# Kernel optimization log

Hardware: AMD Instinct MI355X
Metric: run time of the kernel (lower is better)

## Reference

```python
import jax, jax.numpy as jnp
import numpy as np

B, DIM, H, HD, DS = 256, 1024, 16, 64, 4
NL, NKV = HD, HD * DS  # mask shape constraint: num_tok_q == head_dim, num_tok_kv == head_dim*downscaling
EPS = 1e-5


def _ln(t, g, b):
    m = t.mean(-1, keepdims=True)
    v = ((t - m) ** 2).mean(-1, keepdims=True)
    return (t - m) / jnp.sqrt(v + EPS) * g + b


def setup_inputs() -> dict:
    key = jax.random.key(0)
    ks = jax.random.split(key, 7)
    s = DIM ** -0.5
    return {
        'x': jax.random.normal(ks[0], (B, NKV, DIM), jnp.float32),
        'latents': jax.random.normal(ks[1], (B, NL, DIM), jnp.float32),
        'Wq': jax.random.normal(ks[2], (DIM, DIM), jnp.float32) * s,
        'Wk': jax.random.normal(ks[3], (DIM, DIM), jnp.float32) * s,
        'Wv': jax.random.normal(ks[4], (DIM, DIM), jnp.float32) * s,
        'Wo': jax.random.normal(ks[5], (DIM, DIM), jnp.float32) * s,
        'bo': jnp.zeros((DIM,), jnp.float32),
        'g_out': jnp.ones((DIM,), jnp.float32),
        'b_out': jnp.zeros((DIM,), jnp.float32),
        'g_x': jnp.ones((DIM,), jnp.float32),
        'b_x': jnp.zeros((DIM,), jnp.float32),
        'g_l': jnp.ones((DIM,), jnp.float32),
        'b_l': jnp.zeros((DIM,), jnp.float32),
    }


def reference(x, latents, Wq, Wk, Wv, Wo, bo, g_out, b_out, g_x, b_x, g_l, b_l):
    # pre-norms
    ln_l = _ln(latents, g_l, b_l)   # (B, NL, DIM) -> queries
    ln_x = _ln(x, g_x, b_x)         # (B, NKV, DIM) -> keys/values
    # QKV projections (torch Linear: y = x @ W.T), split heads: b n (h d) -> b h n d
    q = (ln_l @ Wq.T).reshape(B, NL, H, HD).transpose(0, 2, 1, 3)
    k = (ln_x @ Wk.T).reshape(B, NKV, H, HD).transpose(0, 2, 1, 3)
    v = (ln_x @ Wv.T).reshape(B, NKV, H, HD).transpose(0, 2, 1, 3)
    qk = jnp.einsum('bhid,bhjd->bhij', q, k) * (HD ** -0.5)  # (B,H,NL,NKV)
    # faithful to original: (HD,HD) strict-upper -inf mask, repeat_interleave by DS along kv axis
    mask = jnp.triu(jnp.full((HD, HD), -jnp.inf, jnp.float32), k=1)
    mask = jnp.repeat(mask, DS, axis=1)  # (NL, NKV)
    attn = jax.nn.softmax(qk + mask[None, None], axis=-1)
    out = jnp.einsum('bhij,bhjd->bhid', attn, v)
    out = out.transpose(0, 2, 1, 3).reshape(B, NL, DIM)  # b h n d -> b n (h d)
    out = _ln(out, g_out, b_out)      # norm_out (hard-coded True)
    out = out @ Wo.T + bo             # to_out; dropout p=0 -> identity
    return latents + out              # residual=True
```

## Files before the change

kernel.cpp:

```cpp
#include <hip/hip_runtime.h>


typedef unsigned short u16;
typedef float f32x4 __attribute__((ext_vector_type(4)));
typedef short bf16x8 __attribute__((ext_vector_type(8)));
typedef u16 u16x4 __attribute__((ext_vector_type(4)));

#define DEV __device__ __forceinline__

DEV u16 f2bf(float f) {
  union { float f; unsigned int u; } c; c.f = f;
  unsigned int u = c.u;
  u += 0x7fffu + ((u >> 16) & 1u);
  return (u16)(u >> 16);
}
DEV float bf2f(u16 u) {
  union { unsigned int u; float f; } c; c.u = ((unsigned int)u) << 16; return c.f;
}
DEV f32x4 mfma16(bf16x8 a, bf16x8 b, f32x4 c) {
  return __builtin_amdgcn_mfma_f32_16x16x32_bf16(a, b, c, 0, 0, 0);
}
DEV void gl16(const void* g, void* l) {
  __builtin_amdgcn_global_load_lds((const __attribute__((address_space(1))) void*)g,
                                   (__attribute__((address_space(3))) void*)l, 16, 0, 0);
}

template<int INBF>
__global__ __launch_bounds__(256) void ln_kernel(const void* __restrict__ src,
                                                 const float* __restrict__ g,
                                                 const float* __restrict__ bta,
                                                 u16* __restrict__ dst) {
  const int row = blockIdx.x, tid = threadIdx.x;
  float v[4];
  if constexpr (INBF) {
    const u16x4 r = *((const u16x4*)((const u16*)src + (size_t)row * 1024) + tid);
#pragma unroll
    for (int i = 0; i < 4; ++i) v[i] = bf2f(r[i]);
  } else {
    const float4 r = *((const float4*)((const float*)src + (size_t)row * 1024) + tid);
    v[0] = r.x; v[1] = r.y; v[2] = r.z; v[3] = r.w;
  }
  float s = v[0] + v[1] + v[2] + v[3];
  float q = v[0]*v[0] + v[1]*v[1] + v[2]*v[2] + v[3]*v[3];
#pragma unroll
  for (int off = 32; off; off >>= 1) {
    s += __shfl_xor(s, off, 64);
    q += __shfl_xor(q, off, 64);
  }
  __shared__ float red[8];
  if ((tid & 63) == 0) { red[(tid >> 6) * 2] = s; red[(tid >> 6) * 2 + 1] = q; }
  __syncthreads();
  s = red[0] + red[2] + red[4] + red[6];
  q = red[1] + red[3] + red[5] + red[7];
  const float mean = s * (1.f / 1024.f);
  const float rstd = rsqrtf(q * (1.f / 1024.f) - mean * mean + 1e-5f);
  const float4 gv = *((const float4*)g + tid);
  const float4 bv = *((const float4*)bta + tid);
  u16x4 o;
  o[0] = f2bf((v[0] - mean) * rstd * gv.x + bv.x);
  o[1] = f2bf((v[1] - mean) * rstd * gv.y + bv.y);
  o[2] = f2bf((v[2] - mean) * rstd * gv.z + bv.z);
  o[3] = f2bf((v[3] - mean) * rstd * gv.w + bv.w);
  *((u16x4*)(dst + (size_t)row * 1024) + tid) = o;
}

__global__ __launch_bounds__(256) void cvt_kernel(const float* __restrict__ in, u16* __restrict__ out) {
  const int i = (blockIdx.x * 256 + threadIdx.x) * 4;
  const float4 v = *(const float4*)(in + i);
  u16x4 o; o[0] = f2bf(v.x); o[1] = f2bf(v.y); o[2] = f2bf(v.z); o[3] = f2bf(v.w);
  *(u16x4*)(out + i) = o;
}

template<int MODE>
__global__ __launch_bounds__(512, 2) void gemm256(const u16* __restrict__ A,
                                                  const u16* __restrict__ B0,
                                                  const u16* __restrict__ B1,
                                                  u16* __restrict__ o0,
                                                  u16* __restrict__ o1,
                                                  const float* __restrict__ bias,
                                                  const float* __restrict__ resid,
                                                  float* __restrict__ outf,
                                                  int tiles_n) {
  constexpr int NT = 16;
  __shared__ u16 As[2][16384];
  __shared__ u16 Bs[2][16384];
  const int tid = threadIdx.x, lane = tid & 63, wid = tid >> 6;
  const int wm = wid >> 2, wn = wid & 3;
  const int tn = blockIdx.x % tiles_n, tm = blockIdx.x / tiles_n;

  const u16* Asrc = A + (size_t)tm * 256 * 1024;
  const u16* Bsrc;
  if constexpr (MODE == 0)
    Bsrc = (tn < 4) ? (B0 + (size_t)tn * 256 * 1024) : (B1 + (size_t)(tn - 4) * 256 * 1024);
  else
    Bsrc = B0 + (size_t)tn * 256 * 1024;

  int goff[4], loff[4];
#pragma unroll
  for (int i = 0; i < 4; ++i) {
    const int s = i * 512 + tid;
    const int gr = s >> 3, gc = (s & 7) ^ (gr & 7);
    goff[i] = gr * 1024 + gc * 8;
    loff[i] = s * 8;
  }
  const int fr = lane & 15, fq = lane >> 4;
  int chk[2];
#pragma unroll
  for (int ks = 0; ks < 2; ++ks) chk[ks] = ((((ks << 2) + fq)) ^ (lane & 7)) * 8;

  f32x4 acc[8][4];
  const f32x4 z = {0.f, 0.f, 0.f, 0.f};
#pragma unroll
  for (int m = 0; m < 8; ++m)
#pragma unroll
    for (int n = 0; n < 4; ++n) acc[m][n] = z;

#define STG_A(buf, kt, h) { gl16(Asrc + (size_t)(kt) * 64 + goff[2*(h)],     &As[buf][loff[2*(h)]]); \
                            gl16(Asrc + (size_t)(kt) * 64 + goff[2*(h)+1],   &As[buf][loff[2*(h)+1]]); }
#define STG_B(buf, kt, h) { gl16(Bsrc + (size_t)(kt) * 64 + goff[2*(h)],     &Bs[buf][loff[2*(h)]]); \
                            gl16(Bsrc + (size_t)(kt) * 64 + goff[2*(h)+1],   &Bs[buf][loff[2*(h)+1]]); }
#define LDA(H) _Pragma("unroll") for (int mp = 0; mp < 4; ++mp) \
               _Pragma("unroll") for (int ks = 0; ks < 2; ++ks) \
                 af[mp][ks] = *(const bf16x8*)&Ab[(wm * 128 + ((H)*4 + mp) * 16 + fr) * 64 + chk[ks]];
#define LDB(G) _Pragma("unroll") for (int np = 0; np < 2; ++np) \
               _Pragma("unroll") for (int ks = 0; ks < 2; ++ks) \
                 bfr[np][ks] = *(const bf16x8*)&Bb[(wn * 64 + ((G)*2 + np) * 16 + fr) * 64 + chk[ks]];
#define MFMA_Q(H, G) _Pragma("unroll") for (int mp = 0; mp < 4; ++mp) \
                     _Pragma("unroll") for (int np = 0; np < 2; ++np) \
                     _Pragma("unroll") for (int ks = 0; ks < 2; ++ks) \
                       acc[(H)*4 + mp][(G)*2 + np] = mfma16(af[mp][ks], bfr[np][ks], acc[(H)*4 + mp][(G)*2 + np]);

  STG_A(0, 0, 0); STG_A(0, 0, 1);
  STG_B(0, 0, 0); STG_B(0, 0, 1);
  STG_A(1, 1, 0); STG_A(1, 1, 1);
  asm volatile("s_waitcnt vmcnt(4)" ::: "memory");
  __builtin_amdgcn_s_barrier();

  for (int t = 0; t < NT; ++t) {
    const int bsel = t & 1;
    const u16* Ab = As[bsel];
    const u16* Bb = Bs[bsel];
    bf16x8 af[4][2], bfr[2][2];
    LDA(0); LDB(0);
    if (t + 1 < NT) { STG_B(bsel ^ 1, t + 1, 0); STG_B(bsel ^ 1, t + 1, 1); }
    __builtin_amdgcn_s_barrier();
    asm volatile("s_waitcnt lgkmcnt(0)" ::: "memory");
    __builtin_amdgcn_s_setprio(1);
    MFMA_Q(0, 0);
    __builtin_amdgcn_s_setprio(0);
    __builtin_amdgcn_s_barrier();
    LDB(1);
    __builtin_amdgcn_s_barrier();
    asm volatile("s_waitcnt lgkmcnt(0)" ::: "memory");
    __builtin_amdgcn_s_setprio(1);
    MFMA_Q(0, 1);
    __builtin_amdgcn_s_setprio(0);
    __builtin_amdgcn_s_barrier();
    LDA(1);
    __builtin_amdgcn_s_barrier();
    asm volatile("s_waitcnt lgkmcnt(0)" ::: "memory");
    __builtin_amdgcn_s_setprio(1);
    MFMA_Q(1, 1);
    __builtin_amdgcn_s_setprio(0);
    __builtin_amdgcn_s_barrier();
    LDB(0);
    if (t + 2 < NT) { STG_A(bsel, t + 2, 0); STG_A(bsel, t + 2, 1); }
    __builtin_amdgcn_s_barrier();
    asm volatile("s_waitcnt lgkmcnt(0)" ::: "memory");
    __builtin_amdgcn_s_setprio(1);
    MFMA_Q(1, 0);
    __builtin_amdgcn_s_setprio(0);
    if (t + 2 < NT) asm volatile("s_waitcnt vmcnt(4)" ::: "memory");
    else            asm volatile("s_waitcnt vmcnt(0)" ::: "memory");
    __builtin_amdgcn_s_barrier();
  }
#undef STG_A
#undef STG_B
#undef LDA
#undef LDB
#undef MFMA_Q

  if constexpr (MODE == 0) {
    if (tn < 4) {
#pragma unroll
      for (int m = 0; m < 8; ++m) {
        const int t0 = wm * 128 + m * 16 + fq * 4;
#pragma unroll
        for (int n = 0; n < 4; ++n) {
          const int c = tn * 256 + wn * 64 + n * 16 + fr;
          const int h = c >> 6, d = c & 63;
          u16* p = o0 + ((size_t)(tm * 16 + h) * 256 + t0) * 64 + d;
#pragma unroll
          for (int j = 0; j < 4; ++j) p[j * 64] = f2bf(acc[m][n][j]);
        }
      }
    } else {
#pragma unroll
      for (int m = 0; m < 8; ++m) {
        const int t0 = wm * 128 + m * 16 + fq * 4;
#pragma unroll
        for (int n = 0; n < 4; ++n) {
          const int c = (tn - 4) * 256 + wn * 64 + n * 16 + fr;
          const int h = c >> 6, d = c & 63;
          u16x4 o;
#pragma unroll
          for (int j = 0; j < 4; ++j) o[j] = f2bf(acc[m][n][j]);
          *(u16x4*)(o1 + ((size_t)(tm * 16 + h) * 64 + d) * 256 + t0) = o;
        }
      }
    }
  } else if constexpr (MODE == 1) {
#pragma unroll
    for (int m = 0; m < 8; ++m) {
      const int r0 = tm * 256 + wm * 128 + m * 16 + fq * 4;
      const int b = r0 >> 6, i0 = r0 & 63;
#pragma unroll
      for (int n = 0; n < 4; ++n) {
        const int c = tn * 256 + wn * 64 + n * 16 + fr;
        const int h = c >> 6, d = c & 63;
        u16* p = o0 + ((size_t)(b * 16 + h) * 64 + i0) * 64 + d;
#pragma unroll
        for (int j = 0; j < 4; ++j) p[j * 64] = f2bf(acc[m][n][j]);
      }
    }
  } else {
#pragma unroll
    for (int m = 0; m < 8; ++m) {
      const int r0 = tm * 256 + wm * 128 + m * 16 + fq * 4;
#pragma unroll
      for (int n = 0; n < 4; ++n) {
        const int c = tn * 256 + wn * 64 + n * 16 + fr;
        const float bc = bias[c];
#pragma unroll
        for (int j = 0; j < 4; ++j) {
          const size_t idx = (size_t)(r0 + j) * 1024 + c;
          outf[idx] = acc[m][n][j] + bc + resid[idx];
        }
      }
    }
  }
}

__global__ __launch_bounds__(256) void attn_kernel(const u16* __restrict__ Qb,
                                                   const u16* __restrict__ Kb,
                                                   const u16* __restrict__ Vt,
                                                   u16* __restrict__ AO) {
  __shared__ u16 Qs[64 * 64];
  __shared__ u16 Ks[256 * 64];
  __shared__ u16 Vs[64 * 256];
  const int bh = blockIdx.x;
  const int tid = threadIdx.x, lane = tid & 63, wv = tid >> 6;
  const u16* qsrc = Qb + (size_t)bh * 4096;
  const u16* ksrc = Kb + (size_t)bh * 16384;
  const u16* vsrc = Vt + (size_t)bh * 16384;
#pragma unroll
  for (int i = 0; i < 2; ++i) gl16(qsrc + (i * 256 + tid) * 8, &Qs[(i * 256 + tid) * 8]);
#pragma unroll
  for (int i = 0; i < 8; ++i) gl16(ksrc + (i * 256 + tid) * 8, &Ks[(i * 256 + tid) * 8]);
#pragma unroll
  for (int i = 0; i < 8; ++i) gl16(vsrc + (i * 256 + tid) * 8, &Vs[(i * 256 + tid) * 8]);
  __syncthreads();

  f32x4 sacc[16];
  const f32x4 z = {0.f, 0.f, 0.f, 0.f};
#pragma unroll
  for (int n = 0; n < 16; ++n) sacc[n] = z;
#pragma unroll
  for (int s = 0; s < 2; ++s) {
    const bf16x8 aq = *(const bf16x8*)&Qs[(wv * 16 + (lane & 15)) * 64 + s * 32 + (lane >> 4) * 8];
#pragma unroll
    for (int n = 0; n < 16; ++n) {
      const bf16x8 bk = *(const bf16x8*)&Ks[(n * 16 + (lane & 15)) * 64 + s * 32 + (lane >> 4) * 8];
      sacc[n] = mfma16(aq, bk, sacc[n]);
    }
  }

  const int rgrp = lane >> 4, cl = lane & 15;
#pragma unroll
  for (int j = 0; j < 4; ++j) {
    const int qrow = (wv << 4) + (rgrp << 2) + j;
    float m_ = -1e30f;
#pragma unroll
    for (int n = 0; n < 16; ++n) {
      const int col = (n << 4) + cl;
      float sv = sacc[n][j] * 0.125f;
      sv = ((col >> 2) <= qrow) ? sv : -1e30f;
      sacc[n][j] = sv;
      m_ = fmaxf(m_, sv);
    }
#pragma unroll
    for (int off = 8; off; off >>= 1) m_ = fmaxf(m_, __shfl_xor(m_, off, 64));
    float s_ = 0.f;
#pragma unroll
    for (int n = 0; n < 16; ++n) {
      const float p = exp2f((sacc[n][j] - m_) * 1.44269504f);
      sacc[n][j] = p;
      s_ += p;
    }
#pragma unroll
    for (int off = 8; off; off >>= 1) s_ += __shfl_xor(s_, off, 64);
    const float inv = 1.0f / s_;
#pragma unroll
    for (int n = 0; n < 16; ++n) sacc[n][j] *= inv;
  }

  __syncthreads();
  u16* Ps = Ks;
#pragma unroll
  for (int n = 0; n < 16; ++n)
#pragma unroll
    for (int j = 0; j < 4; ++j)
      Ps[((wv << 4) + (rgrp << 2) + j) * 256 + (n << 4) + cl] = f2bf(sacc[n][j]);
  __syncthreads();

  f32x4 oacc[4];
#pragma unroll
  for (int n = 0; n < 4; ++n) oacc[n] = z;
#pragma unroll
  for (int ks = 0; ks < 8; ++ks) {
    const bf16x8 ap = *(const bf16x8*)&Ps[(wv * 16 + (lane & 15)) * 256 + ks * 32 + (lane >> 4) * 8];
#pragma unroll
    for (int n = 0; n < 4; ++n) {
      const bf16x8 bv = *(const bf16x8*)&Vs[(n * 16 + (lane & 15)) * 256 + ks * 32 + (lane >> 4) * 8];
      oacc[n] = mfma16(ap, bv, oacc[n]);
    }
  }
  const int b = bh >> 4, h = bh & 15;
  u16* obase = AO + (size_t)b * 65536 + (size_t)h * 64;
#pragma unroll
  for (int n = 0; n < 4; ++n)
#pragma unroll
    for (int j = 0; j < 4; ++j) {
      const int qrow = (wv << 4) + (rgrp << 2) + j;
      const int d = (n << 4) + cl;
      obase[(size_t)qrow * 1024 + d] = f2bf(oacc[n][j]);
    }
}

extern "C" void kernel_launch(void* const* d_in, const int* in_sizes, int n_in,
                              void* d_out, int out_size, void* d_ws, size_t ws_size,
                              hipStream_t stream) {
  const float* x     = (const float*)d_in[0];
  const float* lat   = (const float*)d_in[1];
  const float* Wq    = (const float*)d_in[2];
  const float* Wk    = (const float*)d_in[3];
  const float* Wv    = (const float*)d_in[4];
  const float* Wo    = (const float*)d_in[5];
  const float* bo    = (const float*)d_in[6];
  const float* g_out = (const float*)d_in[7];
  const float* b_out = (const float*)d_in[8];
  const float* g_x   = (const float*)d_in[9];
  const float* b_x   = (const float*)d_in[10];
  const float* g_l   = (const float*)d_in[11];
  const float* b_l   = (const float*)d_in[12];
  float* out = (float*)d_out;

  char* W = (char*)d_ws;
  u16* wqb = (u16*)(W + 0);
  u16* wkb = (u16*)(W + 2097152);
  u16* wvb = (u16*)(W + 4194304);
  u16* wob = (u16*)(W + 6291456);
  u16* lnl = (u16*)(W + 8388608);
  u16* lnx = (u16*)(W + 41943040);
  u16* qb  = (u16*)(W + 176160768);
  u16* kb  = (u16*)(W + 209715200);
  u16* vt  = (u16*)(W + 343932928);
  u16* ao  = lnx;
  u16* lna = qb;

  cvt_kernel<<<1024, 256, 0, stream>>>(Wq, wqb);
  cvt_kernel<<<1024, 256, 0, stream>>>(Wk, wkb);
  cvt_kernel<<<1024, 256, 0, stream>>>(Wv, wvb);
  cvt_kernel<<<1024, 256, 0, stream>>>(Wo, wob);

  ln_kernel<0><<<16384, 256, 0, stream>>>(lat, g_l, b_l, lnl);
  ln_kernel<0><<<65536, 256, 0, stream>>>(x, g_x, b_x, lnx);

  gemm256<0><<<256 * 8, 512, 0, stream>>>(lnx, wkb, wvb, kb, vt, nullptr, nullptr, nullptr, 8);
  gemm256<1><<<64 * 4, 512, 0, stream>>>(lnl, wqb, nullptr, qb, nullptr, nullptr, nullptr, nullptr, 4);

  attn_kernel<<<4096, 256, 0, stream>>>(qb, kb, vt, ao);

  ln_kernel<1><<<16384, 256, 0, stream>>>(ao, g_out, b_out, lna);

  gemm256<2><<<64 * 4, 512, 0, stream>>>(lna, wob, nullptr, nullptr, nullptr, bo, lat, out, 4);
}
```

Measured before the change: 706.0 us.

## Keep both B fragments in registers, remap GEMM blocks per XCD, fuse weight casts

```diff
diff --git a/kernel.cpp b/kernel.cpp
--- a/kernel.cpp
+++ b/kernel.cpp
@@ -64,11 +64,17 @@
   *((u16x4*)(dst + (size_t)row * 1024) + tid) = o;
 }
 
-__global__ __launch_bounds__(256) void cvt_kernel(const float* __restrict__ in, u16* __restrict__ out) {
-  const int i = (blockIdx.x * 256 + threadIdx.x) * 4;
-  const float4 v = *(const float4*)(in + i);
+__global__ __launch_bounds__(256) void cvt4_kernel(const float* __restrict__ w0,
+                                                   const float* __restrict__ w1,
+                                                   const float* __restrict__ w2,
+                                                   const float* __restrict__ w3,
+                                                   u16* __restrict__ out) {
+  const int g = blockIdx.x >> 10;
+  const float* src = (g == 0) ? w0 : (g == 1) ? w1 : (g == 2) ? w2 : w3;
+  const int i = ((blockIdx.x & 1023) * 256 + threadIdx.x) * 4;
+  const float4 v = *(const float4*)(src + i);
   u16x4 o; o[0] = f2bf(v.x); o[1] = f2bf(v.y); o[2] = f2bf(v.z); o[3] = f2bf(v.w);
-  *(u16x4*)(out + i) = o;
+  *(u16x4*)(out + (size_t)g * 1048576 + i) = o;
 }
 
 template<int MODE>
@@ -86,7 +92,9 @@
   __shared__ u16 Bs[2][16384];
   const int tid = threadIdx.x, lane = tid & 63, wid = tid >> 6;
   const int wm = wid >> 2, wn = wid & 3;
-  const int tn = blockIdx.x % tiles_n, tm = blockIdx.x / tiles_n;
+  const int q8 = (int)gridDim.x >> 3;
+  const int wg = ((int)blockIdx.x & 7) * q8 + ((int)blockIdx.x >> 3);
+  const int tn = wg % tiles_n, tm = wg / tiles_n;
 
   const u16* Asrc = A + (size_t)tm * 256 * 1024;
   const u16* Bsrc;
@@ -122,13 +130,13 @@
 #define LDA(H) _Pragma("unroll") for (int mp = 0; mp < 4; ++mp) \
                _Pragma("unroll") for (int ks = 0; ks < 2; ++ks) \
                  af[mp][ks] = *(const bf16x8*)&Ab[(wm * 128 + ((H)*4 + mp) * 16 + fr) * 64 + chk[ks]];
-#define LDB(G) _Pragma("unroll") for (int np = 0; np < 2; ++np) \
-               _Pragma("unroll") for (int ks = 0; ks < 2; ++ks) \
-                 bfr[np][ks] = *(const bf16x8*)&Bb[(wn * 64 + ((G)*2 + np) * 16 + fr) * 64 + chk[ks]];
-#define MFMA_Q(H, G) _Pragma("unroll") for (int mp = 0; mp < 4; ++mp) \
-                     _Pragma("unroll") for (int np = 0; np < 2; ++np) \
-                     _Pragma("unroll") for (int ks = 0; ks < 2; ++ks) \
-                       acc[(H)*4 + mp][(G)*2 + np] = mfma16(af[mp][ks], bfr[np][ks], acc[(H)*4 + mp][(G)*2 + np]);
+#define LDB(DST, G) _Pragma("unroll") for (int np = 0; np < 2; ++np) \
+                    _Pragma("unroll") for (int ks = 0; ks < 2; ++ks) \
+                      DST[np][ks] = *(const bf16x8*)&Bb[(wn * 64 + ((G)*2 + np) * 16 + fr) * 64 + chk[ks]];
+#define MFMA_Q(H, BF, G) _Pragma("unroll") for (int mp = 0; mp < 4; ++mp) \
+                         _Pragma("unroll") for (int np = 0; np < 2; ++np) \
+                         _Pragma("unroll") for (int ks = 0; ks < 2; ++ks) \
+                           acc[(H)*4 + mp][(G)*2 + np] = mfma16(af[mp][ks], BF[np][ks], acc[(H)*4 + mp][(G)*2 + np]);
 
   STG_A(0, 0, 0); STG_A(0, 0, 1);
   STG_B(0, 0, 0); STG_B(0, 0, 1);
@@ -140,35 +148,33 @@
     const int bsel = t & 1;
     const u16* Ab = As[bsel];
     const u16* Bb = Bs[bsel];
-    bf16x8 af[4][2], bfr[2][2];
-    LDA(0); LDB(0);
-    if (t + 1 < NT) { STG_B(bsel ^ 1, t + 1, 0); STG_B(bsel ^ 1, t + 1, 1); }
+    bf16x8 af[4][2], bfrA[2][2], bfrB[2][2];
+    LDA(0); LDB(bfrA, 0);
+    if (t + 1 < NT) STG_B(bsel ^ 1, t + 1, 0);
     __builtin_amdgcn_s_barrier();
     asm volatile("s_waitcnt lgkmcnt(0)" ::: "memory");
     __builtin_amdgcn_s_setprio(1);
-    MFMA_Q(0, 0);
+    MFMA_Q(0, bfrA, 0);
     __builtin_amdgcn_s_setprio(0);
     __builtin_amdgcn_s_barrier();
-    LDB(1);
+    LDB(bfrB, 1);
+    if (t + 1 < NT) STG_B(bsel ^ 1, t + 1, 1);
     __builtin_amdgcn_s_barrier();
     asm volatile("s_waitcnt lgkmcnt(0)" ::: "memory");
     __builtin_amdgcn_s_setprio(1);
-    MFMA_Q(0, 1);
+    MFMA_Q(0, bfrB, 1);
     __builtin_amdgcn_s_setprio(0);
     __builtin_amdgcn_s_barrier();
     LDA(1);
     __builtin_amdgcn_s_barrier();
     asm volatile("s_waitcnt lgkmcnt(0)" ::: "memory");
     __builtin_amdgcn_s_setprio(1);
-    MFMA_Q(1, 1);
+    MFMA_Q(1, bfrB, 1);
     __builtin_amdgcn_s_setprio(0);
     __builtin_amdgcn_s_barrier();
-    LDB(0);
     if (t + 2 < NT) { STG_A(bsel, t + 2, 0); STG_A(bsel, t + 2, 1); }
-    __builtin_amdgcn_s_barrier();
-    asm volatile("s_waitcnt lgkmcnt(0)" ::: "memory");
     __builtin_amdgcn_s_setprio(1);
-    MFMA_Q(1, 0);
+    MFMA_Q(1, bfrA, 0);
     __builtin_amdgcn_s_setprio(0);
     if (t + 2 < NT) asm volatile("s_waitcnt vmcnt(4)" ::: "memory");
     else            asm volatile("s_waitcnt vmcnt(0)" ::: "memory");
@@ -368,10 +374,7 @@
   u16* ao  = lnx;
   u16* lna = qb;
 
-  cvt_kernel<<<1024, 256, 0, stream>>>(Wq, wqb);
-  cvt_kernel<<<1024, 256, 0, stream>>>(Wk, wkb);
-  cvt_kernel<<<1024, 256, 0, stream>>>(Wv, wvb);
-  cvt_kernel<<<1024, 256, 0, stream>>>(Wo, wob);
+  cvt4_kernel<<<4096, 256, 0, stream>>>(Wq, Wk, Wv, Wo, wqb);
 
   ln_kernel<0><<<16384, 256, 0, stream>>>(lat, g_l, b_l, lnl);
   ln_kernel<0><<<65536, 256, 0, stream>>>(x, g_x, b_x, lnx);
```

Result: faster. 649.3 us (-8.0%).
